# Kernel tuning notes

Measured on AMD Instinct MI355X. Metric: run time of the kernel, lower is better.

Reference implementation:

```python
import jax, jax.numpy as jnp
import numpy as np


def _euler_xyz_to_matrix(angles):
    """pytorch3d euler_angles_to_matrix with convention 'XYZ'.
    angles: [..., 3] -> R = Rx(a0) @ Ry(a1) @ Rz(a2), shape [..., 3, 3]."""
    ax, ay, az = angles[..., 0], angles[..., 1], angles[..., 2]
    cx, sx = jnp.cos(ax), jnp.sin(ax)
    cy, sy = jnp.cos(ay), jnp.sin(ay)
    cz, sz = jnp.cos(az), jnp.sin(az)
    one = jnp.ones_like(cx)
    zero = jnp.zeros_like(cx)
    Rx = jnp.stack([one, zero, zero,
                    zero, cx, -sx,
                    zero, sx, cx], axis=-1).reshape(angles.shape[:-1] + (3, 3))
    Ry = jnp.stack([cy, zero, sy,
                    zero, one, zero,
                    -sy, zero, cy], axis=-1).reshape(angles.shape[:-1] + (3, 3))
    Rz = jnp.stack([cz, -sz, zero,
                    sz, cz, zero,
                    zero, zero, one], axis=-1).reshape(angles.shape[:-1] + (3, 3))
    return Rx @ Ry @ Rz


def setup_inputs() -> dict:
    key = jax.random.key(0)
    k1, k2, k3, k4, k5 = jax.random.split(key, 5)
    B, S, P, V = 16, 16, 64, 2562
    scales = jax.random.uniform(k1, (B, S, 1), dtype=jnp.float32) + 0.5
    transforms = jax.random.normal(k2, (B, S, P, 6), dtype=jnp.float32)
    prototype_weights = jax.random.uniform(k3, (B, S, P), dtype=jnp.float32)
    prototype_offsets = 0.1 * jax.random.normal(k4, (P, V, 3), dtype=jnp.float32)
    bv = jax.random.normal(k5, (V, 3), dtype=jnp.float32)
    base_verts = bv / jnp.linalg.norm(bv, axis=-1, keepdims=True)  # unit sphere
    return {"scales": scales, "transforms": transforms,
            "prototype_weights": prototype_weights,
            "prototype_offsets": prototype_offsets,
            "base_verts": base_verts}


def reference(scales, transforms, prototype_weights, prototype_offsets, base_verts):
    B, S, P = prototype_weights.shape
    V = base_verts.shape[0]
    translation = transforms[..., :3]          # [B,S,P,3]
    rotation = transforms[..., 3:]             # [B,S,P,3]
    R = _euler_xyz_to_matrix(rotation)         # [B,S,P,3,3]
    deformed = base_verts[None] + prototype_offsets  # [P,V,3]
    # per-(b,s,p): out += w * (scale * (deformed @ R^T) + t)
    # fold weight*scale into R, reduce over p in one contraction
    ws = prototype_weights * scales            # [B,S,P]
    Rws = R * ws[..., None, None]              # [B,S,P,3,3]
    rotated = jnp.einsum('bspij,pvj->bsvi', Rws, deformed)  # [B,S,V,3]
    trans = jnp.einsum('bsp,bspi->bsi', prototype_weights, translation)  # [B,S,3]
    out = rotated + trans[:, :, None, :]       # [B,S,V,3]
    return out.reshape(B * S, V, 3)
```

## Files before the change

kernel.cpp:

```cpp
#include <hip/hip_runtime.h>

#define NP 64
#define NV 2562
#define NVP 2576
#define KK 192
#define NT 161
#define MQ 16

typedef short bf16x8 __attribute__((ext_vector_type(8)));
typedef float f32x4  __attribute__((ext_vector_type(4)));

static __device__ __forceinline__ unsigned short f2bf(float x) {
    unsigned u = __float_as_uint(x);
    return (unsigned short)((u + 0x7fffu + ((u >> 16) & 1u)) >> 16);
}


__global__ __launch_bounds__(64) void prep_a_kernel(
    const float* __restrict__ scales,
    const float* __restrict__ transforms,
    const float* __restrict__ weights,
    unsigned short* __restrict__ A,
    float* __restrict__ aux)
{
    const int bs = blockIdx.x;
    const int p  = threadIdx.x;

    const float* t = transforms + ((size_t)bs * NP + p) * 6;
    const float tx = t[0], ty = t[1], tz = t[2];
    const float ax = t[3], ay = t[4], az = t[5];
    const float w  = weights[bs * NP + p];
    const float sc = scales[bs];
    const float ws = w * sc;

    float sx, cx, sy, cy, sz, cz;
    __sincosf(ax, &sx, &cx);
    __sincosf(ay, &sy, &cy);
    __sincosf(az, &sz, &cz);

    float v12[12];
    v12[0] = (cy * cz) * ws;
    v12[1] = (-cy * sz) * ws;
    v12[2] = (sy) * ws;
    v12[3] = (cx * sz + sx * sy * cz) * ws;
    v12[4] = (cx * cz - sx * sy * sz) * ws;
    v12[5] = (-sx * cy) * ws;
    v12[6] = (sx * sz - cx * sy * cz) * ws;
    v12[7] = (sx * cz + cx * sy * sz) * ws;
    v12[8] = (cx * cy) * ws;
    v12[9]  = w * tx;
    v12[10] = w * ty;
    v12[11] = w * tz;

#pragma unroll
    for (int i = 0; i < 3; ++i) {
        unsigned short* row = A + ((size_t)(bs * 4 + i)) * KK + p * 3;
        row[0] = f2bf(v12[i * 3 + 0]);
        row[1] = f2bf(v12[i * 3 + 1]);
        row[2] = f2bf(v12[i * 3 + 2]);
    }

    float red[12];
#pragma unroll
    for (int k = 0; k < 12; ++k) red[k] = v12[k];
#pragma unroll
    for (int m = 1; m < 64; m <<= 1) {
#pragma unroll
        for (int k = 0; k < 12; ++k) red[k] += __shfl_xor(red[k], m);
    }
    if (p == 0) {
#pragma unroll
        for (int k = 0; k < 12; ++k) aux[bs * 12 + k] = red[k];
    }
}

__global__ __launch_bounds__(128) void prep_b_kernel(
    const float* __restrict__ offsets,
    unsigned short* __restrict__ Bt)
{
    const int v = blockIdx.x * 128 + threadIdx.x;
    if (v >= NVP) return;
    const int p0 = blockIdx.y * 2;

    float o[6] = {0, 0, 0, 0, 0, 0};
    if (v < NV) {
        const float* a = offsets + ((size_t)p0 * NV + v) * 3;
        const float* b = offsets + ((size_t)(p0 + 1) * NV + v) * 3;
        o[0] = a[0]; o[1] = a[1]; o[2] = a[2];
        o[3] = b[0]; o[4] = b[1]; o[5] = b[2];
    }
    unsigned w0 = (unsigned)f2bf(o[0]) | ((unsigned)f2bf(o[1]) << 16);
    unsigned w1 = (unsigned)f2bf(o[2]) | ((unsigned)f2bf(o[3]) << 16);
    unsigned w2 = (unsigned)f2bf(o[4]) | ((unsigned)f2bf(o[5]) << 16);
    unsigned* dst = (unsigned*)(Bt + (size_t)v * KK + p0 * 3);
    dst[0] = w0; dst[1] = w1; dst[2] = w2;
}

__global__ __launch_bounds__(256) void gemm_kernel(
    const unsigned short* __restrict__ A,
    const unsigned short* __restrict__ Bt,
    const float* __restrict__ aux,
    const float* __restrict__ bverts,
    float* __restrict__ out)
{
    __shared__ float tile[4][16][17];

    const int t    = threadIdx.x;
    const int wave = t >> 6;
    const int lane = t & 63;
    const int q    = lane >> 4;
    const int r16  = lane & 15;

    const int nt = blockIdx.x;
    const int mt = blockIdx.y * 4 + wave;
    const int n0 = nt * 16;

    const int am = mt * 16 + r16;
    const int bn = n0 + r16;

    const unsigned short* ap = A  + (size_t)am * KK + q * 8;
    const unsigned short* bp = Bt + (size_t)bn * KK + q * 8;

    f32x4 acc = {0.f, 0.f, 0.f, 0.f};
#pragma unroll
    for (int ks = 0; ks < 6; ++ks) {
        bf16x8 a = *(const bf16x8*)(ap + ks * 32);
        bf16x8 b = *(const bf16x8*)(bp + ks * 32);
        acc = __builtin_amdgcn_mfma_f32_16x16x32_bf16(a, b, acc, 0, 0, 0);
    }

#pragma unroll
    for (int rg = 0; rg < 4; ++rg)
        tile[wave][q * 4 + rg][r16] = acc[rg];

    const int a_i  = lane % 3;
    const int vloc = lane / 3;
    const int v    = n0 + vloc;
    const int vc   = v < NV ? v : NV - 1;

    const float bx = bverts[vc * 3 + 0];
    const float by = bverts[vc * 3 + 1];
    const float bz = bverts[vc * 3 + 2];

    const int bs_base = mt * 4;
#pragma unroll
    for (int bi = 0; bi < 4; ++bi) {
        const int bs = bs_base + bi;
        const float* ax = aux + bs * 12;
        float val = tile[wave][bi * 4 + a_i][vloc];
        val += ax[a_i * 3 + 0] * bx + ax[a_i * 3 + 1] * by + ax[a_i * 3 + 2] * bz
             + ax[9 + a_i];
        if (lane < 48 && v < NV)
            out[(size_t)bs * NV * 3 + n0 * 3 + lane] = val;
    }
}

extern "C" void kernel_launch(void* const* d_in, const int* in_sizes, int n_in,
                              void* d_out, int out_size, void* d_ws, size_t ws_size,
                              hipStream_t stream) {
    const float* scales     = (const float*)d_in[0];
    const float* transforms = (const float*)d_in[1];
    const float* weights    = (const float*)d_in[2];
    const float* offsets    = (const float*)d_in[3];
    const float* bverts     = (const float*)d_in[4];
    float* out = (float*)d_out;

    unsigned short* A  = (unsigned short*)d_ws;
    unsigned short* Bt = A + (size_t)1024 * KK;
    float* aux = (float*)(Bt + (size_t)NVP * KK);

    prep_a_kernel<<<dim3(256), dim3(64), 0, stream>>>(scales, transforms, weights, A, aux);
    prep_b_kernel<<<dim3((NVP + 127) / 128, NP / 2), dim3(128), 0, stream>>>(offsets, Bt);
    gemm_kernel<<<dim3(NT, MQ), dim3(256), 0, stream>>>(A, Bt, aux, bverts, out);
}
```

Before: 87.82 us.

## Fuse prep kernels into single GEMM kernel with LDS-staged A and B tiles

Merges the two preprocessing kernels into the GEMM kernel: each block builds its 16 batch rows of A (rotation matrices via sincos) and a 32-vertex slice of B (bf16 offsets) directly in LDS, then runs MFMA from LDS. A rows are padded to 4 per batch (the fourth zeroed), so each accumulator lane directly holds the xyz triple for one vertex and can write output without the shared-memory transpose. This removes two launches and the global workspace round trip. In exchange, A is recomputed redundantly by each of the 81 column blocks, and B is re-converted by each of the 16 row blocks.

```diff
diff --git a/kernel.cpp b/kernel.cpp
--- a/kernel.cpp
+++ b/kernel.cpp
@@ -2,10 +2,11 @@
 
 #define NP 64
 #define NV 2562
-#define NVP 2576
 #define KK 192
-#define NT 161
-#define MQ 16
+#define STR 200
+#define NVB 32
+#define GX 81
+#define GY 16
 
 typedef short bf16x8 __attribute__((ext_vector_type(8)));
 typedef float f32x4  __attribute__((ext_vector_type(4)));
@@ -15,143 +16,143 @@
     return (unsigned short)((u + 0x7fffu + ((u >> 16) & 1u)) >> 16);
 }
 
-
-__global__ __launch_bounds__(64) void prep_a_kernel(
+__global__ __launch_bounds__(256) void fused_gemm_kernel(
     const float* __restrict__ scales,
     const float* __restrict__ transforms,
     const float* __restrict__ weights,
-    unsigned short* __restrict__ A,
-    float* __restrict__ aux)
-{
-    const int bs = blockIdx.x;
-    const int p  = threadIdx.x;
-
-    const float* t = transforms + ((size_t)bs * NP + p) * 6;
-    const float tx = t[0], ty = t[1], tz = t[2];
-    const float ax = t[3], ay = t[4], az = t[5];
-    const float w  = weights[bs * NP + p];
-    const float sc = scales[bs];
-    const float ws = w * sc;
-
-    float sx, cx, sy, cy, sz, cz;
-    __sincosf(ax, &sx, &cx);
-    __sincosf(ay, &sy, &cy);
-    __sincosf(az, &sz, &cz);
-
-    float v12[12];
-    v12[0] = (cy * cz) * ws;
-    v12[1] = (-cy * sz) * ws;
-    v12[2] = (sy) * ws;
-    v12[3] = (cx * sz + sx * sy * cz) * ws;
-    v12[4] = (cx * cz - sx * sy * sz) * ws;
-    v12[5] = (-sx * cy) * ws;
-    v12[6] = (sx * sz - cx * sy * cz) * ws;
-    v12[7] = (sx * cz + cx * sy * sz) * ws;
-    v12[8] = (cx * cy) * ws;
-    v12[9]  = w * tx;
-    v12[10] = w * ty;
-    v12[11] = w * tz;
-
-#pragma unroll
-    for (int i = 0; i < 3; ++i) {
-        unsigned short* row = A + ((size_t)(bs * 4 + i)) * KK + p * 3;
-        row[0] = f2bf(v12[i * 3 + 0]);
-        row[1] = f2bf(v12[i * 3 + 1]);
-        row[2] = f2bf(v12[i * 3 + 2]);
-    }
-
-    float red[12];
-#pragma unroll
-    for (int k = 0; k < 12; ++k) red[k] = v12[k];
-#pragma unroll
-    for (int m = 1; m < 64; m <<= 1) {
-#pragma unroll
-        for (int k = 0; k < 12; ++k) red[k] += __shfl_xor(red[k], m);
-    }
-    if (p == 0) {
-#pragma unroll
-        for (int k = 0; k < 12; ++k) aux[bs * 12 + k] = red[k];
-    }
-}
-
-__global__ __launch_bounds__(128) void prep_b_kernel(
     const float* __restrict__ offsets,
-    unsigned short* __restrict__ Bt)
-{
-    const int v = blockIdx.x * 128 + threadIdx.x;
-    if (v >= NVP) return;
-    const int p0 = blockIdx.y * 2;
-
-    float o[6] = {0, 0, 0, 0, 0, 0};
-    if (v < NV) {
-        const float* a = offsets + ((size_t)p0 * NV + v) * 3;
-        const float* b = offsets + ((size_t)(p0 + 1) * NV + v) * 3;
-        o[0] = a[0]; o[1] = a[1]; o[2] = a[2];
-        o[3] = b[0]; o[4] = b[1]; o[5] = b[2];
-    }
-    unsigned w0 = (unsigned)f2bf(o[0]) | ((unsigned)f2bf(o[1]) << 16);
-    unsigned w1 = (unsigned)f2bf(o[2]) | ((unsigned)f2bf(o[3]) << 16);
-    unsigned w2 = (unsigned)f2bf(o[4]) | ((unsigned)f2bf(o[5]) << 16);
-    unsigned* dst = (unsigned*)(Bt + (size_t)v * KK + p0 * 3);
-    dst[0] = w0; dst[1] = w1; dst[2] = w2;
-}
-
-__global__ __launch_bounds__(256) void gemm_kernel(
-    const unsigned short* __restrict__ A,
-    const unsigned short* __restrict__ Bt,
-    const float* __restrict__ aux,
     const float* __restrict__ bverts,
     float* __restrict__ out)
 {
-    __shared__ float tile[4][16][17];
+    __shared__ unsigned short Alds[64][STR];
+    __shared__ unsigned short Blds[NVB][STR];
+    __shared__ float saux[16][12];
 
-    const int t    = threadIdx.x;
-    const int wave = t >> 6;
+    const int t   = threadIdx.x;
+    const int n0  = blockIdx.x * NVB;
+    const int bs0 = blockIdx.y * 16;
+
+    {
+        const int p  = t >> 2;
+        const int vg = (t & 3) * 8;
+#pragma unroll
+        for (int v8 = 0; v8 < 8; ++v8) {
+            const int vloc = vg + v8;
+            const int v    = n0 + vloc;
+            const int vc   = v < NV ? v : NV - 1;
+            const float* o = offsets + ((size_t)p * NV + vc) * 3;
+            Blds[vloc][p * 3 + 0] = f2bf(o[0]);
+            Blds[vloc][p * 3 + 1] = f2bf(o[1]);
+            Blds[vloc][p * 3 + 2] = f2bf(o[2]);
+        }
+    }
+
+    {
+        const int w = t >> 6;
+        const int p = t & 63;
+#pragma unroll
+        for (int j = 0; j < 4; ++j) {
+            const int bs = bs0 + w * 4 + j;
+            const float sc = scales[bs];
+            const float* tr = transforms + ((size_t)bs * NP + p) * 6;
+            const float tx = tr[0], ty = tr[1], tz = tr[2];
+            const float ax = tr[3], ay = tr[4], az = tr[5];
+            const float wgt = weights[bs * NP + p];
+            const float ws  = wgt * sc;
+
+            float sx, cx, sy, cy, sz, cz;
+            __sincosf(ax, &sx, &cx);
+            __sincosf(ay, &sy, &cy);
+            __sincosf(az, &sz, &cz);
+
+            float v12[12];
+            v12[0] = (cy * cz) * ws;
+            v12[1] = (-cy * sz) * ws;
+            v12[2] = (sy) * ws;
+            v12[3] = (cx * sz + sx * sy * cz) * ws;
+            v12[4] = (cx * cz - sx * sy * sz) * ws;
+            v12[5] = (-sx * cy) * ws;
+            v12[6] = (sx * sz - cx * sy * cz) * ws;
+            v12[7] = (sx * cz + cx * sy * sz) * ws;
+            v12[8] = (cx * cy) * ws;
+            v12[9]  = wgt * tx;
+            v12[10] = wgt * ty;
+            v12[11] = wgt * tz;
+
+            const int r0 = w * 16 + j * 4;
+#pragma unroll
+            for (int i = 0; i < 3; ++i) {
+                Alds[r0 + i][p * 3 + 0] = f2bf(v12[i * 3 + 0]);
+                Alds[r0 + i][p * 3 + 1] = f2bf(v12[i * 3 + 1]);
+                Alds[r0 + i][p * 3 + 2] = f2bf(v12[i * 3 + 2]);
+            }
+            Alds[r0 + 3][p * 3 + 0] = 0;
+            Alds[r0 + 3][p * 3 + 1] = 0;
+            Alds[r0 + 3][p * 3 + 2] = 0;
+
+            float red[12];
+#pragma unroll
+            for (int k = 0; k < 12; ++k) red[k] = v12[k];
+#pragma unroll
+            for (int m = 1; m < 64; m <<= 1) {
+#pragma unroll
+                for (int k = 0; k < 12; ++k) red[k] += __shfl_xor(red[k], m);
+            }
+            if (p == 0) {
+#pragma unroll
+                for (int k = 0; k < 12; ++k) saux[w * 4 + j][k] = red[k];
+            }
+        }
+    }
+    __syncthreads();
+
+    const int w    = t >> 6;
     const int lane = t & 63;
     const int q    = lane >> 4;
     const int r16  = lane & 15;
 
-    const int nt = blockIdx.x;
-    const int mt = blockIdx.y * 4 + wave;
-    const int n0 = nt * 16;
+    const unsigned short* ap  = &Alds[w * 16 + r16][q * 8];
+    const unsigned short* bp0 = &Blds[r16][q * 8];
+    const unsigned short* bp1 = &Blds[16 + r16][q * 8];
 
-    const int am = mt * 16 + r16;
-    const int bn = n0 + r16;
-
-    const unsigned short* ap = A  + (size_t)am * KK + q * 8;
-    const unsigned short* bp = Bt + (size_t)bn * KK + q * 8;
-
-    f32x4 acc = {0.f, 0.f, 0.f, 0.f};
+    f32x4 acc0 = {0.f, 0.f, 0.f, 0.f};
+    f32x4 acc1 = {0.f, 0.f, 0.f, 0.f};
 #pragma unroll
     for (int ks = 0; ks < 6; ++ks) {
-        bf16x8 a = *(const bf16x8*)(ap + ks * 32);
-        bf16x8 b = *(const bf16x8*)(bp + ks * 32);
-        acc = __builtin_amdgcn_mfma_f32_16x16x32_bf16(a, b, acc, 0, 0, 0);
+        bf16x8 a  = *(const bf16x8*)(ap  + ks * 32);
+        bf16x8 b0 = *(const bf16x8*)(bp0 + ks * 32);
+        bf16x8 b1 = *(const bf16x8*)(bp1 + ks * 32);
+        acc0 = __builtin_amdgcn_mfma_f32_16x16x32_bf16(a, b0, acc0, 0, 0, 0);
+        acc1 = __builtin_amdgcn_mfma_f32_16x16x32_bf16(a, b1, acc1, 0, 0, 0);
     }
 
+    const int bsl = w * 4 + q;
+    float R[12];
 #pragma unroll
-    for (int rg = 0; rg < 4; ++rg)
-        tile[wave][q * 4 + rg][r16] = acc[rg];
+    for (int k = 0; k < 12; ++k) R[k] = saux[bsl][k];
 
-    const int a_i  = lane % 3;
-    const int vloc = lane / 3;
-    const int v    = n0 + vloc;
-    const int vc   = v < NV ? v : NV - 1;
-
-    const float bx = bverts[vc * 3 + 0];
-    const float by = bverts[vc * 3 + 1];
-    const float bz = bverts[vc * 3 + 2];
-
-    const int bs_base = mt * 4;
-#pragma unroll
-    for (int bi = 0; bi < 4; ++bi) {
-        const int bs = bs_base + bi;
-        const float* ax = aux + bs * 12;
-        float val = tile[wave][bi * 4 + a_i][vloc];
-        val += ax[a_i * 3 + 0] * bx + ax[a_i * 3 + 1] * by + ax[a_i * 3 + 2] * bz
-             + ax[9 + a_i];
-        if (lane < 48 && v < NV)
-            out[(size_t)bs * NV * 3 + n0 * 3 + lane] = val;
+    const int bs = bs0 + bsl;
+    {
+        const int v = n0 + r16;
+        if (v < NV) {
+            const float bx = bverts[v * 3 + 0];
+            const float by = bverts[v * 3 + 1];
+            const float bz = bverts[v * 3 + 2];
+            float* po = out + ((size_t)bs * NV + v) * 3;
+            po[0] = acc0[0] + R[0] * bx + R[1] * by + R[2] * bz + R[9];
+            po[1] = acc0[1] + R[3] * bx + R[4] * by + R[5] * bz + R[10];
+            po[2] = acc0[2] + R[6] * bx + R[7] * by + R[8] * bz + R[11];
+        }
+        const int v1 = n0 + 16 + r16;
+        if (v1 < NV) {
+            const float bx = bverts[v1 * 3 + 0];
+            const float by = bverts[v1 * 3 + 1];
+            const float bz = bverts[v1 * 3 + 2];
+            float* po = out + ((size_t)bs * NV + v1) * 3;
+            po[0] = acc1[0] + R[0] * bx + R[1] * by + R[2] * bz + R[9];
+            po[1] = acc1[1] + R[3] * bx + R[4] * by + R[5] * bz + R[10];
+            po[2] = acc1[2] + R[6] * bx + R[7] * by + R[8] * bz + R[11];
+        }
     }
 }
 
@@ -165,11 +166,6 @@
     const float* bverts     = (const float*)d_in[4];
     float* out = (float*)d_out;
 
-    unsigned short* A  = (unsigned short*)d_ws;
-    unsigned short* Bt = A + (size_t)1024 * KK;
-    float* aux = (float*)(Bt + (size_t)NVP * KK);
-
-    prep_a_kernel<<<dim3(256), dim3(64), 0, stream>>>(scales, transforms, weights, A, aux);
-    prep_b_kernel<<<dim3((NVP + 127) / 128, NP / 2), dim3(128), 0, stream>>>(offsets, Bt);
-    gemm_kernel<<<dim3(NT, MQ), dim3(256), 0, stream>>>(A, Bt, aux, bverts, out);
+    fused_gemm_kernel<<<dim3(GX, GY), dim3(256), 0, stream>>>(
+        scales, transforms, weights, offsets, bverts, out);
 }
```

Measured after the change: 105.8 us. 1.2x slower.
